# Kernel tuning notes

Hardware: AMD Instinct MI355X
Metric: run time of the kernel (lower is better)

## Reference

```python
import jax, jax.numpy as jnp
import numpy as np

# Kernel codes matching style 'L;O2;P2;Y2,1,1;R0.5;W1,1'
KERNEL_CODES = ['L', 'O', 'P', 'Y', 'R', 'W']
SM_TEMP = 1.0


def _norm_sq(q, k):
    # q: [n,l,h,e], k: [n,s,h,e] -> [n,h,l,s]
    q2 = jnp.einsum('nlhe,nlhe->nhl', q, q)[..., None]        # [n,h,l,1]
    k2 = jnp.einsum('nshe,nshe->nhs', k, k)[:, :, None, :]     # [n,h,1,s]
    qk = jnp.einsum('nlhe,nshe->nhls', q, k)
    return q2 + k2 - 2.0 * qk


def _kernel(code, q, k):
    if code == 'L':
        return jnp.einsum('nlhe,nshe->nhls', q, k)
    if code == 'O':  # -log(1 + ns^(p/2)), p=2
        return -jnp.log1p(_norm_sq(q, k))
    if code == 'P':  # -(ns)^(p/2), p=2
        return -_norm_sq(q, k)
    if code == 'Y':  # (alpha*<q,k> + c)^p, p=2, alpha=1, c=1
        d = jnp.einsum('nlhe,nshe->nhls', q, k)
        return (d + 1.0) ** 2
    if code == 'R':  # exp(-gamma*ns), gamma=0.5
        return jnp.exp(-0.5 * _norm_sq(q, k))
    if code == 'W':  # cos(ns/a)*exp(-ns/b), a=b=1
        ns = _norm_sq(q, k)
        return jnp.cos(ns) * jnp.exp(-ns)
    raise ValueError(code)


def setup_inputs() -> dict:
    key = jax.random.key(0)
    k1, k2, k3, k4 = jax.random.split(key, 4)
    N, L, S, H, E, K = 2, 1024, 1024, 8, 64, 6
    return {
        'query': jax.random.normal(k1, (N, L, H, E), dtype=jnp.float32),
        'key': jax.random.normal(k2, (N, S, H, E), dtype=jnp.float32),
        'attn_mask_add': jnp.zeros((N, L, S), dtype=jnp.float32),
        'key_lengths_add': jnp.zeros((N, S), dtype=jnp.float32),
        'M': jax.random.uniform(k3, (H, E, K), dtype=jnp.float32),
        'C': jax.random.uniform(k4, (K, H, E, E), dtype=jnp.float32),
    }


def reference(query, key, attn_mask_add, key_lengths_add, M, C):
    # mixture weights pi: [n,l,h,k]
    pi = jax.nn.softmax(jnp.einsum('nlhe,hek->nlhk', query, M), axis=-1)
    out = None
    for c, code in enumerate(KERNEL_CODES):
        # htilde = tanh(query @ C[c]): [n,l,h,e]
        htilde = jnp.tanh(jnp.einsum('nlhe,hef->nlhf', query, C[c]))
        qk = _kernel(code, htilde, key)                    # [n,h,l,s]
        qk = qk + attn_mask_add[:, None] + key_lengths_add[:, None, None, :]
        sm = jax.nn.softmax(SM_TEMP * qk, axis=-1)
        w = jnp.transpose(pi[..., c], (0, 2, 1))[..., None]  # [n,h,l,1]
        term = sm * w
        out = term if out is None else out + term
    return out
```

## Files before the change

kernel.cpp:

```cpp
#include <hip/hip_runtime.h>
#include <hip/hip_bf16.h>
#include <math.h>

#define N_  2
#define H_  8
#define G_  16
#define L_  1024
#define S_  1024
#define E_  64
#define NC_ 6

typedef __attribute__((ext_vector_type(4))) float floatx4;
typedef __attribute__((ext_vector_type(8))) short short8;

#define MFMA16 __builtin_amdgcn_mfma_f32_16x16x32_bf16

#define AHAT_OFF   0
#define AHAT_BYTES (NC_*G_*L_*128*2)
#define KHAT_OFF   (AHAT_OFF + AHAT_BYTES)
#define KHAT_BYTES (G_*S_*128*2)
#define PI_OFF     (KHAT_OFF + KHAT_BYTES)
#define PI_BYTES   (NC_*G_*L_*4)
#define HSQ_OFF    (PI_OFF + PI_BYTES)
#define HSQ_BYTES  (NC_*G_*L_*4)
#define KSQ_OFF    (HSQ_OFF + HSQ_BYTES)
#define KSQ_BYTES  (G_*S_*4)

__device__ __forceinline__ float ftanh(float x) {
  return 1.0f - 2.0f * __builtin_amdgcn_rcpf(__expf(2.0f*x) + 1.0f);
}

__global__ __launch_bounds__(256) void k_prep(
    const float* __restrict__ q, const float* __restrict__ C,
    const float* __restrict__ key, const float* __restrict__ M,
    __hip_bfloat16* __restrict__ Ahat, float* __restrict__ hsq,
    __hip_bfloat16* __restrict__ Khat, float* __restrict__ ksq,
    float* __restrict__ pi_t) {
  __shared__ float Ms[384];
  const int bx = blockIdx.x;
  const int t = threadIdx.x;
  const int w = t >> 6, lane = t & 63;
  const int quad = lane >> 4, lc = lane & 15;

  if (bx < 512) {
    const int g = bx >> 5, lch = bx & 31;
    const int n = g >> 3, h = g & 7;
    const int lt = lch*32 + (w >> 1)*16;
    const int c0 = (w & 1)*3;

    short8 qh[2], ql[2];
    #pragma unroll
    for (int kc = 0; kc < 2; kc++) {
      const float* qp = q + (((size_t)(n*L_ + lt + lc))*H_ + h)*E_ + kc*32 + quad*8;
      float4 a0 = *(const float4*)qp, a1 = *(const float4*)(qp + 4);
      float v[8] = {a0.x,a0.y,a0.z,a0.w,a1.x,a1.y,a1.z,a1.w};
      #pragma unroll
      for (int j = 0; j < 8; j++) {
        __hip_bfloat16 hb = __float2bfloat16(v[j]);
        __hip_bfloat16 lb = __float2bfloat16(v[j] - __bfloat162float(hb));
        short hs, ls;
        __builtin_memcpy(&hs, &hb, 2); __builtin_memcpy(&ls, &lb, 2);
        qh[kc][j] = hs; ql[kc][j] = ls;
      }
    }

    #pragma unroll 1
    for (int cc = 0; cc < 3; cc++) {
      const int c = c0 + cc;
      const float* Cb = C + ((size_t)(c*8 + h))*64*64;
      float ss[4] = {0.f, 0.f, 0.f, 0.f};
      #pragma unroll 2
      for (int ft = 0; ft < 4; ft++) {
        short8 bh[2], bl[2];
        #pragma unroll
        for (int kc = 0; kc < 2; kc++)
          #pragma unroll
          for (int j = 0; j < 8; j++) {
            float cv = Cb[(size_t)(kc*32 + quad*8 + j)*64 + ft*16 + lc];
            __hip_bfloat16 hb = __float2bfloat16(cv);
            __hip_bfloat16 lb = __float2bfloat16(cv - __bfloat162float(hb));
            short hs, ls;
            __builtin_memcpy(&hs, &hb, 2); __builtin_memcpy(&ls, &lb, 2);
            bh[kc][j] = hs; bl[kc][j] = ls;
          }
        floatx4 d = {0.f, 0.f, 0.f, 0.f};
        d = MFMA16(qh[0], bh[0], d, 0,0,0);
        d = MFMA16(qh[1], bh[1], d, 0,0,0);
        d = MFMA16(qh[0], bl[0], d, 0,0,0);
        d = MFMA16(qh[1], bl[1], d, 0,0,0);
        d = MFMA16(ql[0], bh[0], d, 0,0,0);
        d = MFMA16(ql[1], bh[1], d, 0,0,0);
        #pragma unroll
        for (int i = 0; i < 4; i++) {
          float hv = ftanh(d[i]);
          ss[i] += hv*hv;
          __hip_bfloat16 hb = __float2bfloat16(hv);
          __hip_bfloat16 lb = __float2bfloat16(hv - __bfloat162float(hb));
          char* rowp = (char*)Ahat +
              (((size_t)(c*G_ + g))*L_ + lt + quad*4 + i)*256;
          *(__hip_bfloat16*)(rowp + (ft*16 + lc)*2)       = hb;
          *(__hip_bfloat16*)(rowp + 128 + (ft*16 + lc)*2) = lb;
        }
      }
      #pragma unroll
      for (int i = 0; i < 4; i++) {
        float s = ss[i];
        s += __shfl_xor(s, 1); s += __shfl_xor(s, 2);
        s += __shfl_xor(s, 4); s += __shfl_xor(s, 8);
        if (lc == 0) hsq[((size_t)(c*G_ + g))*L_ + lt + quad*4 + i] = s;
      }
    }
  } else if (bx < 768) {
    const int kb = bx - 512;
    #pragma unroll 2
    for (int it = 0; it < 16; it++) {
      int r = kb*64 + it*4 + w;
      int kg = r >> 10, s = r & 1023, kn = kg >> 3, kh = kg & 7;
      float v = key[(((size_t)(kn*S_ + s))*H_ + kh)*E_ + lane];
      __hip_bfloat16 hi = __float2bfloat16(v);
      __hip_bfloat16 lo = __float2bfloat16(v - __bfloat162float(hi));
      size_t base = ((size_t)kg*S_ + s)*128;
      Khat[base + lane]      = hi;
      Khat[base + 64 + lane] = lo;
      float sq = v*v;
      #pragma unroll
      for (int off = 32; off; off >>= 1) sq += __shfl_xor(sq, off);
      if (lane == 0) ksq[(size_t)kg*S_ + s] = sq;
    }
  } else {
    const int pb = bx - 768;
    const int pg = pb >> 2, lch = pb & 3;
    const int pn = pg >> 3, ph = pg & 7;
    const int l = lch*256 + t;
    for (int u = t; u < 384; u += 256) Ms[u] = M[ph*384 + u];
    __syncthreads();
    const float* qrow = q + (((size_t)(pn*L_ + l))*H_ + ph)*E_;
    float p[6] = {0.f, 0.f, 0.f, 0.f, 0.f, 0.f};
    #pragma unroll 8
    for (int e = 0; e < 64; e++) {
      float qv = qrow[e];
      #pragma unroll
      for (int k = 0; k < 6; k++) p[k] = fmaf(qv, Ms[e*6 + k], p[k]);
    }
    float mx = p[0];
    #pragma unroll
    for (int k = 1; k < 6; k++) mx = fmaxf(mx, p[k]);
    float den = 0.f;
    #pragma unroll
    for (int k = 0; k < 6; k++) den += __expf(p[k] - mx);
    float rden = __builtin_amdgcn_rcpf(den);
    #pragma unroll
    for (int k = 0; k < 6; k++)
      pi_t[((size_t)(k*G_ + pg))*L_ + l] = __expf(p[k] - mx) * rden;
  }
}

#define LDS_A6LO  0
#define LDS_ZRED  13824
#define LDS_MRED  15360
#define LDS_CST   16896
#define LDS_TOTAL 17664

__global__ __launch_bounds__(256, 2) void k_main(
    const __hip_bfloat16* __restrict__ Ahat, const __hip_bfloat16* __restrict__ Khat,
    const float* __restrict__ hsq, const float* __restrict__ ksq,
    const float* __restrict__ mask, const float* __restrict__ klen,
    const float* __restrict__ pi_t, float* __restrict__ out) {
  extern __shared__ char smraw[];
  char*   A6     = smraw + LDS_A6LO;
  float*  zred   = (float*)(smraw + LDS_ZRED);
  float*  mred   = (float*)(smraw + LDS_MRED);
  float2* cst    = (float2*)(smraw + LDS_CST);

  const int l0 = blockIdx.x * 16; const int g = blockIdx.y; const int n = g >> 3;
  const int t = threadIdx.x; const int w = t >> 6; const int lane = t & 63;
  const int quad = lane >> 4; const int lc = lane & 15;

  #pragma unroll
  for (int rep = 0; rep < 3; rep++) {
    int u = t + rep*256; int row = u >> 3, seg = u & 7;
    int cc = row >> 4, lr = row & 15;
    *(int4*)(A6 + row*144 + seg*16) =
      *(const int4*)((const char*)Ahat +
          (((size_t)(cc*G_ + g))*L_ + l0 + lr)*256 + 128 + seg*16);
  }

  short8 ah[6][2];
  #pragma unroll
  for (int cc = 0; cc < 6; cc++) {
    const char* arow = (const char*)Ahat + (((size_t)(cc*G_ + g))*L_ + l0 + lc)*256;
    ah[cc][0] = *(const short8*)(arow + quad*16);
    ah[cc][1] = *(const short8*)(arow + 64 + quad*16);
  }

  float h1p = 1.0f  + hsq[((size_t)(1*G_ + g))*L_ + l0 + lc];
  float nh2 = 64.0f - hsq[((size_t)(2*G_ + g))*L_ + l0 + lc];
  float h4h = -0.5f * hsq[((size_t)(4*G_ + g))*L_ + l0 + lc];
  float nh5 = -hsq[((size_t)(5*G_ + g))*L_ + l0 + lc];

  __syncthreads();

  auto LOADK = [&](int st, short8 (&bf)[4]) {
    const char* base = (const char*)Khat +
        (((size_t)g)*S_ + st*64 + w*16 + lc)*256 + quad*16;
    #pragma unroll
    for (int kt = 0; kt < 4; kt++)
      bf[kt] = *(const short8*)(base + kt*64);
  };

  float Zc0 = 0.f, Zc1 = 0.f, Zc2 = 0.f, Zc3 = 0.f, zp = 0.f;
  float m3 = -INFINITY, z3 = 0.f;

  auto SWEEP1 = [&](int st, const short8 (&bf)[4]) {
    int sb = st*64 + w*16 + quad*4;
    float4 mk4 = *(const float4*)(mask + ((size_t)(n*L_ + l0 + lc))*S_ + sb);
    float4 kl4 = *(const float4*)(klen + (size_t)n*S_ + sb);
    float4 kq4 = *(const float4*)(ksq  + (size_t)g*S_ + sb);
    float kq[4] = {kq4.x, kq4.y, kq4.z, kq4.w};
    float mv[4], Ev[4];
    mv[0] = mk4.x + kl4.x; mv[1] = mk4.y + kl4.y;
    mv[2] = mk4.z + kl4.z; mv[3] = mk4.w + kl4.w;
    #pragma unroll
    for (int i = 0; i < 4; i++) Ev[i] = __expf(mv[i]);
    #pragma unroll
    for (int c = 0; c < 6; c++) {
      short8 al0 = *(const short8*)(A6 + (c*16 + lc)*144 + quad*16);
      short8 al1 = *(const short8*)(A6 + (c*16 + lc)*144 + 64 + quad*16);
      floatx4 a = {0.f, 0.f, 0.f, 0.f};
      a = MFMA16(bf[0], ah[c][0], a, 0,0,0);
      a = MFMA16(bf[1], ah[c][1], a, 0,0,0);
      a = MFMA16(bf[0], al0,      a, 0,0,0);
      a = MFMA16(bf[1], al1,      a, 0,0,0);
      a = MFMA16(bf[2], ah[c][0], a, 0,0,0);
      a = MFMA16(bf[3], ah[c][1], a, 0,0,0);
      #pragma unroll
      for (int i = 0; i < 4; i++) {
        float d = a[i];
        if (c == 0) {
          Zc0 = fmaf(Ev[i], __expf(d), Zc0);
        } else if (c == 1) {
          Zc1 = fmaf(Ev[i], __builtin_amdgcn_rcpf(fmaf(-2.f, d, h1p + kq[i])), Zc1);
        } else if (c == 2) {
          zp += __expf(fmaf(2.f, d, nh2 - kq[i] + mv[i]));
        } else if (c == 3) {
          float tt = d + 1.f;
          float x  = fmaf(tt, tt, mv[i]);
          float mn = fmaxf(m3, x);
          float e  = __expf(fminf(m3, x) - mn);
          z3 = (x > m3) ? fmaf(z3, e, 1.0f) : (z3 + e);
          m3 = mn;
        } else if (c == 4) {
          Zc2 = fmaf(Ev[i], __expf(__expf(d + fmaf(-0.5f, kq[i], h4h))), Zc2);
        } else {
          float a5 = fmaf(2.f, d, nh5 - kq[i]);
          Zc3 = fmaf(Ev[i], __expf(__cosf(a5) * __expf(a5)), Zc3);
        }
      }
    }
  };

  {
    short8 bA[4], bB[4];
    LOADK(0, bA);
    #pragma unroll 1
    for (int st = 0; st < 16; st += 2) {
      LOADK(st + 1, bB);
      SWEEP1(st, bA);
      LOADK((st + 2) & 15, bA);
      SWEEP1(st + 1, bB);
    }
  }

  #pragma unroll
  for (int off = 16; off < 64; off <<= 1) {
    Zc0 += __shfl_xor(Zc0, off); Zc1 += __shfl_xor(Zc1, off);
    Zc2 += __shfl_xor(Zc2, off); Zc3 += __shfl_xor(Zc3, off);
    zp  += __shfl_xor(zp,  off);
    float mo = __shfl_xor(m3, off);
    float zo = __shfl_xor(z3, off);
    float mn = fmaxf(m3, mo);
    float e  = __expf(fminf(m3, mo) - mn);
    z3 = (mo > m3) ? fmaf(z3, e, zo) : fmaf(zo, e, z3);
    m3 = mn;
  }
  if (lane < 16) {
    zred[w*96 + 0*16 + lc] = Zc0; mred[w*96 + 0*16 + lc] = 0.f;
    zred[w*96 + 1*16 + lc] = Zc1; mred[w*96 + 1*16 + lc] = 0.f;
    zred[w*96 + 2*16 + lc] = zp;  mred[w*96 + 2*16 + lc] = 0.f;
    zred[w*96 + 3*16 + lc] = z3;  mred[w*96 + 3*16 + lc] = m3;
    zred[w*96 + 4*16 + lc] = Zc2; mred[w*96 + 4*16 + lc] = 0.f;
    zred[w*96 + 5*16 + lc] = Zc3; mred[w*96 + 5*16 + lc] = 0.f;
  }
  __syncthreads();
  if (t < 96) {
    int c = t >> 4;
    float z = zred[t], m = mred[t];
    if (c == 3) {
      #pragma unroll
      for (int w2 = 1; w2 < 4; w2++) {
        float mo = mred[w2*96 + t], zo = zred[w2*96 + t];
        float mn = fmaxf(m, mo);
        float e  = __expf(fminf(m, mo) - mn);
        z = (mo > m) ? fmaf(z, e, zo) : fmaf(zo, e, z);
        m = mn;
      }
    } else {
      #pragma unroll
      for (int w2 = 1; w2 < 4; w2++) z += zred[w2*96 + t];
    }
    float piv = pi_t[((size_t)((t >> 4)*G_ + g))*L_ + l0 + (t & 15)];
    cst[t] = make_float2(piv / z, m);
  }
  __syncthreads();

  float ac0 = cst[0*16 + lc].x, ac1 = cst[1*16 + lc].x, ac2 = cst[2*16 + lc].x;
  float ac3 = cst[3*16 + lc].x, ac4 = cst[4*16 + lc].x, ac5 = cst[5*16 + lc].x;
  float m3f = cst[3*16 + lc].y;

  auto SWEEP2 = [&](int st, const short8 (&bf)[4]) {
    int sb = st*64 + w*16 + quad*4;
    float4 mk4 = *(const float4*)(mask + ((size_t)(n*L_ + l0 + lc))*S_ + sb);
    float4 kl4 = *(const float4*)(klen + (size_t)n*S_ + sb);
    float4 kq4 = *(const float4*)(ksq  + (size_t)g*S_ + sb);
    float kq[4] = {kq4.x, kq4.y, kq4.z, kq4.w};
    float mv[4], Ev[4];
    mv[0] = mk4.x + kl4.x; mv[1] = mk4.y + kl4.y;
    mv[2] = mk4.z + kl4.z; mv[3] = mk4.w + kl4.w;
    #pragma unroll
    for (int i = 0; i < 4; i++) Ev[i] = __expf(mv[i]);
    float Sacc[4] = {0.f, 0.f, 0.f, 0.f};
    float Gg[4]   = {0.f, 0.f, 0.f, 0.f};
    #pragma unroll
    for (int c = 0; c < 6; c++) {
      short8 al0 = *(const short8*)(A6 + (c*16 + lc)*144 + quad*16);
      short8 al1 = *(const short8*)(A6 + (c*16 + lc)*144 + 64 + quad*16);
      floatx4 a = {0.f, 0.f, 0.f, 0.f};
      a = MFMA16(bf[0], ah[c][0], a, 0,0,0);
      a = MFMA16(bf[1], ah[c][1], a, 0,0,0);
      a = MFMA16(bf[0], al0,      a, 0,0,0);
      a = MFMA16(bf[1], al1,      a, 0,0,0);
      a = MFMA16(bf[2], ah[c][0], a, 0,0,0);
      a = MFMA16(bf[3], ah[c][1], a, 0,0,0);
      #pragma unroll
      for (int i = 0; i < 4; i++) {
        float d = a[i];
        if (c == 0) {
          Sacc[i] = fmaf(ac0, __expf(d), Sacc[i]);
        } else if (c == 1) {
          Sacc[i] = fmaf(ac1, __builtin_amdgcn_rcpf(fmaf(-2.f, d, h1p + kq[i])), Sacc[i]);
        } else if (c == 2) {
          Gg[i] = fmaf(ac2, __expf(fmaf(2.f, d, nh2 - kq[i] + mv[i])), Gg[i]);
        } else if (c == 3) {
          float tt = d + 1.f;
          float x  = fmaf(tt, tt, mv[i]);
          Gg[i] = fmaf(ac3, __expf(x - m3f), Gg[i]);
        } else if (c == 4) {
          Sacc[i] = fmaf(ac4, __expf(__expf(d + fmaf(-0.5f, kq[i], h4h))), Sacc[i]);
        } else {
          float a5 = fmaf(2.f, d, nh5 - kq[i]);
          Sacc[i] = fmaf(ac5, __expf(__cosf(a5) * __expf(a5)), Sacc[i]);
        }
      }
    }
    float4 ov;
    ov.x = fmaf(Ev[0], Sacc[0], Gg[0]);
    ov.y = fmaf(Ev[1], Sacc[1], Gg[1]);
    ov.z = fmaf(Ev[2], Sacc[2], Gg[2]);
    ov.w = fmaf(Ev[3], Sacc[3], Gg[3]);
    *(float4*)(out + (((size_t)g)*L_ + l0 + lc)*S_ + sb) = ov;
  };

  {
    short8 bA[4], bB[4];
    LOADK(0, bA);
    #pragma unroll 1
    for (int st = 0; st < 16; st += 2) {
      LOADK(st + 1, bB);
      SWEEP2(st, bA);
      LOADK((st + 2) & 15, bA);
      SWEEP2(st + 1, bB);
    }
  }
}

extern "C" void kernel_launch(void* const* d_in, const int* in_sizes, int n_in,
                              void* d_out, int out_size, void* d_ws, size_t ws_size,
                              hipStream_t stream) {
  (void)in_sizes; (void)n_in; (void)out_size; (void)ws_size;
  const float* q    = (const float*)d_in[0];
  const float* key  = (const float*)d_in[1];
  const float* mask = (const float*)d_in[2];
  const float* klen = (const float*)d_in[3];
  const float* M    = (const float*)d_in[4];
  const float* C    = (const float*)d_in[5];
  char* ws = (char*)d_ws;
  __hip_bfloat16* Ahat = (__hip_bfloat16*)(ws + AHAT_OFF);
  __hip_bfloat16* Khat = (__hip_bfloat16*)(ws + KHAT_OFF);
  float* pi_t    = (float*)(ws + PI_OFF);
  float* hsq     = (float*)(ws + HSQ_OFF);
  float* ksq     = (float*)(ws + KSQ_OFF);
  float* out = (float*)d_out;

  k_prep<<<832, 256, 0, stream>>>(q, C, key, M, Ahat, hsq, Khat, ksq, pi_t);
  k_main<<<dim3(64, 16), 256, LDS_TOTAL, stream>>>(Ahat, Khat, hsq, ksq, mask, klen,
                                                   pi_t, out);
}
```

Measured before the change: 207.2 us.

## Move A hi/lo fragments to LDS, premerge mask+klen, raise occupancy to three blocks

The hi bf16 query fragments now live in LDS together with the lo parts, which frees registers, and launch bounds go from 2 to 3 blocks per CU. A new prep stage precomputes mask+key_length into a workspace buffer, so the main kernel does one load instead of two and folds the additive mask into the exponent instead of multiplying by exp(mask). The K-tile double buffer is replaced by a single buffer that is prefetched after the last MFMA. The costs are extra LDS reads per tile, an extra 8 MB write and read of the merged mask, and less latency hiding from the single buffer.

```diff
diff --git a/kernel.cpp b/kernel.cpp
--- a/kernel.cpp
+++ b/kernel.cpp
@@ -25,6 +25,8 @@
 #define HSQ_BYTES  (NC_*G_*L_*4)
 #define KSQ_OFF    (HSQ_OFF + HSQ_BYTES)
 #define KSQ_BYTES  (G_*S_*4)
+#define MKL_OFF    (KSQ_OFF + KSQ_BYTES)
+#define MKL_BYTES  (N_*L_*S_*4)
 
 __device__ __forceinline__ float ftanh(float x) {
   return 1.0f - 2.0f * __builtin_amdgcn_rcpf(__expf(2.0f*x) + 1.0f);
@@ -33,9 +35,10 @@
 __global__ __launch_bounds__(256) void k_prep(
     const float* __restrict__ q, const float* __restrict__ C,
     const float* __restrict__ key, const float* __restrict__ M,
+    const float* __restrict__ mask, const float* __restrict__ klen,
     __hip_bfloat16* __restrict__ Ahat, float* __restrict__ hsq,
     __hip_bfloat16* __restrict__ Khat, float* __restrict__ ksq,
-    float* __restrict__ pi_t) {
+    float* __restrict__ pi_t, float* __restrict__ mkl) {
   __shared__ float Ms[384];
   const int bx = blockIdx.x;
   const int t = threadIdx.x;
@@ -127,7 +130,7 @@
       for (int off = 32; off; off >>= 1) sq += __shfl_xor(sq, off);
       if (lane == 0) ksq[(size_t)kg*S_ + s] = sq;
     }
-  } else {
+  } else if (bx < 832) {
     const int pb = bx - 768;
     const int pg = pb >> 2, lch = pb & 3;
     const int pn = pg >> 3, ph = pg & 7;
@@ -152,45 +155,49 @@
     #pragma unroll
     for (int k = 0; k < 6; k++)
       pi_t[((size_t)(k*G_ + pg))*L_ + l] = __expf(p[k] - mx) * rden;
+  } else {
+    const int mb = bx - 832;
+    const float4* m4 = (const float4*)mask;
+    const float4* k4 = (const float4*)klen;
+    float4* o4 = (float4*)mkl;
+    #pragma unroll 1
+    for (int u = mb*256 + t; u < N_*L_*S_/4; u += 128*256) {
+      int nn = u >> 18;
+      int s4 = u & 255;
+      float4 a = m4[u], b = k4[nn*256 + s4];
+      o4[u] = make_float4(a.x+b.x, a.y+b.y, a.z+b.z, a.w+b.w);
+    }
   }
 }
 
-#define LDS_A6LO  0
-#define LDS_ZRED  13824
-#define LDS_MRED  15360
-#define LDS_CST   16896
-#define LDS_TOTAL 17664
-
-__global__ __launch_bounds__(256, 2) void k_main(
+#define LDS_A6    0
+#define LDS_ZRED  26112
+#define LDS_MRED  27648
+#define LDS_CST   29184
+#define LDS_TOTAL 29952
+
+__global__ __launch_bounds__(256, 3) void k_main(
     const __hip_bfloat16* __restrict__ Ahat, const __hip_bfloat16* __restrict__ Khat,
     const float* __restrict__ hsq, const float* __restrict__ ksq,
-    const float* __restrict__ mask, const float* __restrict__ klen,
-    const float* __restrict__ pi_t, float* __restrict__ out) {
+    const float* __restrict__ mkl, const float* __restrict__ pi_t,
+    float* __restrict__ out) {
   extern __shared__ char smraw[];
-  char*   A6     = smraw + LDS_A6LO;
-  float*  zred   = (float*)(smraw + LDS_ZRED);
-  float*  mred   = (float*)(smraw + LDS_MRED);
-  float2* cst    = (float2*)(smraw + LDS_CST);
+  char*   A6   = smraw + LDS_A6;
+  float*  zred = (float*)(smraw + LDS_ZRED);
+  float*  mred = (float*)(smraw + LDS_MRED);
+  float2* cst  = (float2*)(smraw + LDS_CST);
 
   const int l0 = blockIdx.x * 16; const int g = blockIdx.y; const int n = g >> 3;
   const int t = threadIdx.x; const int w = t >> 6; const int lane = t & 63;
   const int quad = lane >> 4; const int lc = lane & 15;
 
   #pragma unroll
-  for (int rep = 0; rep < 3; rep++) {
-    int u = t + rep*256; int row = u >> 3, seg = u & 7;
+  for (int rep = 0; rep < 6; rep++) {
+    int u = t + rep*256; int row = u >> 4, seg = u & 15;
     int cc = row >> 4, lr = row & 15;
-    *(int4*)(A6 + row*144 + seg*16) =
+    *(int4*)(A6 + row*272 + seg*16) =
       *(const int4*)((const char*)Ahat +
-          (((size_t)(cc*G_ + g))*L_ + l0 + lr)*256 + 128 + seg*16);
-  }
-
-  short8 ah[6][2];
-  #pragma unroll
-  for (int cc = 0; cc < 6; cc++) {
-    const char* arow = (const char*)Ahat + (((size_t)(cc*G_ + g))*L_ + l0 + lc)*256;
-    ah[cc][0] = *(const short8*)(arow + quad*16);
-    ah[cc][1] = *(const short8*)(arow + 64 + quad*16);
+          (((size_t)(cc*G_ + g))*L_ + l0 + lr)*256 + seg*16);
   }
 
   float h1p = 1.0f  + hsq[((size_t)(1*G_ + g))*L_ + l0 + lc];
@@ -211,63 +218,56 @@
   float Zc0 = 0.f, Zc1 = 0.f, Zc2 = 0.f, Zc3 = 0.f, zp = 0.f;
   float m3 = -INFINITY, z3 = 0.f;
 
-  auto SWEEP1 = [&](int st, const short8 (&bf)[4]) {
-    int sb = st*64 + w*16 + quad*4;
-    float4 mk4 = *(const float4*)(mask + ((size_t)(n*L_ + l0 + lc))*S_ + sb);
-    float4 kl4 = *(const float4*)(klen + (size_t)n*S_ + sb);
-    float4 kq4 = *(const float4*)(ksq  + (size_t)g*S_ + sb);
-    float kq[4] = {kq4.x, kq4.y, kq4.z, kq4.w};
-    float mv[4], Ev[4];
-    mv[0] = mk4.x + kl4.x; mv[1] = mk4.y + kl4.y;
-    mv[2] = mk4.z + kl4.z; mv[3] = mk4.w + kl4.w;
-    #pragma unroll
-    for (int i = 0; i < 4; i++) Ev[i] = __expf(mv[i]);
-    #pragma unroll
-    for (int c = 0; c < 6; c++) {
-      short8 al0 = *(const short8*)(A6 + (c*16 + lc)*144 + quad*16);
-      short8 al1 = *(const short8*)(A6 + (c*16 + lc)*144 + 64 + quad*16);
-      floatx4 a = {0.f, 0.f, 0.f, 0.f};
-      a = MFMA16(bf[0], ah[c][0], a, 0,0,0);
-      a = MFMA16(bf[1], ah[c][1], a, 0,0,0);
-      a = MFMA16(bf[0], al0,      a, 0,0,0);
-      a = MFMA16(bf[1], al1,      a, 0,0,0);
-      a = MFMA16(bf[2], ah[c][0], a, 0,0,0);
-      a = MFMA16(bf[3], ah[c][1], a, 0,0,0);
-      #pragma unroll
-      for (int i = 0; i < 4; i++) {
-        float d = a[i];
-        if (c == 0) {
-          Zc0 = fmaf(Ev[i], __expf(d), Zc0);
-        } else if (c == 1) {
-          Zc1 = fmaf(Ev[i], __builtin_amdgcn_rcpf(fmaf(-2.f, d, h1p + kq[i])), Zc1);
-        } else if (c == 2) {
-          zp += __expf(fmaf(2.f, d, nh2 - kq[i] + mv[i]));
-        } else if (c == 3) {
-          float tt = d + 1.f;
-          float x  = fmaf(tt, tt, mv[i]);
-          float mn = fmaxf(m3, x);
-          float e  = __expf(fminf(m3, x) - mn);
-          z3 = (x > m3) ? fmaf(z3, e, 1.0f) : (z3 + e);
-          m3 = mn;
-        } else if (c == 4) {
-          Zc2 = fmaf(Ev[i], __expf(__expf(d + fmaf(-0.5f, kq[i], h4h))), Zc2);
-        } else {
-          float a5 = fmaf(2.f, d, nh5 - kq[i]);
-          Zc3 = fmaf(Ev[i], __expf(__cosf(a5) * __expf(a5)), Zc3);
+  {
+    short8 bf[4];
+    LOADK(0, bf);
+    #pragma unroll 1
+    for (int st = 0; st < 16; st++) {
+      int sb = st*64 + w*16 + quad*4;
+      float4 mv4 = *(const float4*)(mkl + ((size_t)(n*L_ + l0 + lc))*S_ + sb);
+      float4 kq4 = *(const float4*)(ksq + (size_t)g*S_ + sb);
+      float mv[4] = {mv4.x, mv4.y, mv4.z, mv4.w};
+      float kq[4] = {kq4.x, kq4.y, kq4.z, kq4.w};
+      #pragma unroll
+      for (int c = 0; c < 6; c++) {
+        const char* Ar = A6 + (c*16 + lc)*272 + quad*16;
+        short8 h0  = *(const short8*)(Ar);
+        short8 h1  = *(const short8*)(Ar + 64);
+        short8 al0 = *(const short8*)(Ar + 128);
+        short8 al1 = *(const short8*)(Ar + 192);
+        floatx4 a = {0.f, 0.f, 0.f, 0.f};
+        a = MFMA16(bf[0], h0,  a, 0,0,0);
+        a = MFMA16(bf[1], h1,  a, 0,0,0);
+        a = MFMA16(bf[0], al0, a, 0,0,0);
+        a = MFMA16(bf[1], al1, a, 0,0,0);
+        a = MFMA16(bf[2], h0,  a, 0,0,0);
+        a = MFMA16(bf[3], h1,  a, 0,0,0);
+        if (c == 5) LOADK((st + 1) & 15, bf);
+        #pragma unroll
+        for (int i = 0; i < 4; i++) {
+          float d = a[i];
+          if (c == 0) {
+            Zc0 += __expf(d + mv[i]);
+          } else if (c == 1) {
+            Zc1 = fmaf(__expf(mv[i]),
+                __builtin_amdgcn_rcpf(fmaf(-2.f, d, h1p + kq[i])), Zc1);
+          } else if (c == 2) {
+            zp += __expf(fmaf(2.f, d, nh2 - kq[i] + mv[i]));
+          } else if (c == 3) {
+            float tt = d + 1.f;
+            float x  = fmaf(tt, tt, mv[i]);
+            float mn = fmaxf(m3, x);
+            float e  = __expf(fminf(m3, x) - mn);
+            z3 = (x > m3) ? fmaf(z3, e, 1.0f) : (z3 + e);
+            m3 = mn;
+          } else if (c == 4) {
+            Zc2 += __expf(__expf(d + fmaf(-0.5f, kq[i], h4h)) + mv[i]);
+          } else {
+            float a5 = fmaf(2.f, d, nh5 - kq[i]);
+            Zc3 += __expf(fmaf(__cosf(a5), __expf(a5), mv[i]));
+          }
         }
       }
-    }
-  };
-
-  {
-    short8 bA[4], bB[4];
-    LOADK(0, bA);
-    #pragma unroll 1
-    for (int st = 0; st < 16; st += 2) {
-      LOADK(st + 1, bB);
-      SWEEP1(st, bA);
-      LOADK((st + 2) & 15, bA);
-      SWEEP1(st + 1, bB);
     }
   }
 
@@ -317,68 +317,57 @@
   float ac3 = cst[3*16 + lc].x, ac4 = cst[4*16 + lc].x, ac5 = cst[5*16 + lc].x;
   float m3f = cst[3*16 + lc].y;
 
-  auto SWEEP2 = [&](int st, const short8 (&bf)[4]) {
-    int sb = st*64 + w*16 + quad*4;
-    float4 mk4 = *(const float4*)(mask + ((size_t)(n*L_ + l0 + lc))*S_ + sb);
-    float4 kl4 = *(const float4*)(klen + (size_t)n*S_ + sb);
-    float4 kq4 = *(const float4*)(ksq  + (size_t)g*S_ + sb);
-    float kq[4] = {kq4.x, kq4.y, kq4.z, kq4.w};
-    float mv[4], Ev[4];
-    mv[0] = mk4.x + kl4.x; mv[1] = mk4.y + kl4.y;
-    mv[2] = mk4.z + kl4.z; mv[3] = mk4.w + kl4.w;
-    #pragma unroll
-    for (int i = 0; i < 4; i++) Ev[i] = __expf(mv[i]);
-    float Sacc[4] = {0.f, 0.f, 0.f, 0.f};
-    float Gg[4]   = {0.f, 0.f, 0.f, 0.f};
-    #pragma unroll
-    for (int c = 0; c < 6; c++) {
-      short8 al0 = *(const short8*)(A6 + (c*16 + lc)*144 + quad*16);
-      short8 al1 = *(const short8*)(A6 + (c*16 + lc)*144 + 64 + quad*16);
-      floatx4 a = {0.f, 0.f, 0.f, 0.f};
-      a = MFMA16(bf[0], ah[c][0], a, 0,0,0);
-      a = MFMA16(bf[1], ah[c][1], a, 0,0,0);
-      a = MFMA16(bf[0], al0,      a, 0,0,0);
-      a = MFMA16(bf[1], al1,      a, 0,0,0);
-      a = MFMA16(bf[2], ah[c][0], a, 0,0,0);
-      a = MFMA16(bf[3], ah[c][1], a, 0,0,0);
-      #pragma unroll
-      for (int i = 0; i < 4; i++) {
-        float d = a[i];
-        if (c == 0) {
-          Sacc[i] = fmaf(ac0, __expf(d), Sacc[i]);
-        } else if (c == 1) {
-          Sacc[i] = fmaf(ac1, __builtin_amdgcn_rcpf(fmaf(-2.f, d, h1p + kq[i])), Sacc[i]);
-        } else if (c == 2) {
-          Gg[i] = fmaf(ac2, __expf(fmaf(2.f, d, nh2 - kq[i] + mv[i])), Gg[i]);
-        } else if (c == 3) {
-          float tt = d + 1.f;
-          float x  = fmaf(tt, tt, mv[i]);
-          Gg[i] = fmaf(ac3, __expf(x - m3f), Gg[i]);
-        } else if (c == 4) {
-          Sacc[i] = fmaf(ac4, __expf(__expf(d + fmaf(-0.5f, kq[i], h4h))), Sacc[i]);
-        } else {
-          float a5 = fmaf(2.f, d, nh5 - kq[i]);
-          Sacc[i] = fmaf(ac5, __expf(__cosf(a5) * __expf(a5)), Sacc[i]);
+  {
+    short8 bf[4];
+    LOADK(0, bf);
+    #pragma unroll 1
+    for (int st = 0; st < 16; st++) {
+      int sb = st*64 + w*16 + quad*4;
+      float4 mv4 = *(const float4*)(mkl + ((size_t)(n*L_ + l0 + lc))*S_ + sb);
+      float4 kq4 = *(const float4*)(ksq + (size_t)g*S_ + sb);
+      float mv[4] = {mv4.x, mv4.y, mv4.z, mv4.w};
+      float kq[4] = {kq4.x, kq4.y, kq4.z, kq4.w};
+      float Gg[4] = {0.f, 0.f, 0.f, 0.f};
+      #pragma unroll
+      for (int c = 0; c < 6; c++) {
+        const char* Ar = A6 + (c*16 + lc)*272 + quad*16;
+        short8 h0  = *(const short8*)(Ar);
+        short8 h1  = *(const short8*)(Ar + 64);
+        short8 al0 = *(const short8*)(Ar + 128);
+        short8 al1 = *(const short8*)(Ar + 192);
+        floatx4 a = {0.f, 0.f, 0.f, 0.f};
+        a = MFMA16(bf[0], h0,  a, 0,0,0);
+        a = MFMA16(bf[1], h1,  a, 0,0,0);
+        a = MFMA16(bf[0], al0, a, 0,0,0);
+        a = MFMA16(bf[1], al1, a, 0,0,0);
+        a = MFMA16(bf[2], h0,  a, 0,0,0);
+        a = MFMA16(bf[3], h1,  a, 0,0,0);
+        if (c == 5) LOADK((st + 1) & 15, bf);
+        #pragma unroll
+        for (int i = 0; i < 4; i++) {
+          float d = a[i];
+          if (c == 0) {
+            Gg[i] = fmaf(ac0, __expf(d + mv[i]), Gg[i]);
+          } else if (c == 1) {
+            Gg[i] = fmaf(ac1 * __expf(mv[i]),
+                __builtin_amdgcn_rcpf(fmaf(-2.f, d, h1p + kq[i])), Gg[i]);
+          } else if (c == 2) {
+            Gg[i] = fmaf(ac2, __expf(fmaf(2.f, d, nh2 - kq[i] + mv[i])), Gg[i]);
+          } else if (c == 3) {
+            float tt = d + 1.f;
+            Gg[i] = fmaf(ac3, __expf(fmaf(tt, tt, mv[i]) - m3f), Gg[i]);
+          } else if (c == 4) {
+            Gg[i] = fmaf(ac4,
+                __expf(__expf(d + fmaf(-0.5f, kq[i], h4h)) + mv[i]), Gg[i]);
+          } else {
+            float a5 = fmaf(2.f, d, nh5 - kq[i]);
+            Gg[i] = fmaf(ac5, __expf(fmaf(__cosf(a5), __expf(a5), mv[i])), Gg[i]);
+          }
         }
       }
-    }
-    float4 ov;
-    ov.x = fmaf(Ev[0], Sacc[0], Gg[0]);
-    ov.y = fmaf(Ev[1], Sacc[1], Gg[1]);
-    ov.z = fmaf(Ev[2], Sacc[2], Gg[2]);
-    ov.w = fmaf(Ev[3], Sacc[3], Gg[3]);
-    *(float4*)(out + (((size_t)g)*L_ + l0 + lc)*S_ + sb) = ov;
-  };
-
-  {
-    short8 bA[4], bB[4];
-    LOADK(0, bA);
-    #pragma unroll 1
-    for (int st = 0; st < 16; st += 2) {
-      LOADK(st + 1, bB);
-      SWEEP2(st, bA);
-      LOADK((st + 2) & 15, bA);
-      SWEEP2(st + 1, bB);
+      float4 ov;
+      ov.x = Gg[0]; ov.y = Gg[1]; ov.z = Gg[2]; ov.w = Gg[3];
+      *(float4*)(out + (((size_t)g)*L_ + l0 + lc)*S_ + sb) = ov;
     }
   }
 }
@@ -399,9 +388,11 @@
   float* pi_t    = (float*)(ws + PI_OFF);
   float* hsq     = (float*)(ws + HSQ_OFF);
   float* ksq     = (float*)(ws + KSQ_OFF);
+  float* mkl     = (float*)(ws + MKL_OFF);
   float* out = (float*)d_out;
 
-  k_prep<<<832, 256, 0, stream>>>(q, C, key, M, Ahat, hsq, Khat, ksq, pi_t);
-  k_main<<<dim3(64, 16), 256, LDS_TOTAL, stream>>>(Ahat, Khat, hsq, ksq, mask, klen,
+  k_prep<<<960, 256, 0, stream>>>(q, C, key, M, mask, klen,
+                                  Ahat, hsq, Khat, ksq, pi_t, mkl);
+  k_main<<<dim3(64, 16), 256, LDS_TOTAL, stream>>>(Ahat, Khat, hsq, ksq, mkl,
                                                    pi_t, out);
 }
```

After: 221.0 us. 6.7% more time.

## Precombine mask and key-length bias in prep and prefetch them with key tiles

Applied to the files above, without the earlier changes.

Adds a prep stage that sums attn_mask and key_lengths into an mkl buffer, so the main kernel reads one bias array instead of two. The bias and ksq loads are now software-pipelined alongside the K tile prefetch. Each wave also starts its S sweep at a different tile offset, which spreads concurrent accesses across memory. The cost is an extra 8MB write and read through the workspace in the prep kernel, to save one small load and an add per element in the two main sweeps.

```diff
diff --git a/kernel.cpp b/kernel.cpp
--- a/kernel.cpp
+++ b/kernel.cpp
@@ -25,6 +25,8 @@
 #define HSQ_BYTES  (NC_*G_*L_*4)
 #define KSQ_OFF    (HSQ_OFF + HSQ_BYTES)
 #define KSQ_BYTES  (G_*S_*4)
+#define MKL_OFF    (KSQ_OFF + KSQ_BYTES)
+#define MKL_BYTES  (N_*L_*S_*4)
 
 __device__ __forceinline__ float ftanh(float x) {
   return 1.0f - 2.0f * __builtin_amdgcn_rcpf(__expf(2.0f*x) + 1.0f);
@@ -33,9 +35,10 @@
 __global__ __launch_bounds__(256) void k_prep(
     const float* __restrict__ q, const float* __restrict__ C,
     const float* __restrict__ key, const float* __restrict__ M,
+    const float* __restrict__ mask, const float* __restrict__ klen,
     __hip_bfloat16* __restrict__ Ahat, float* __restrict__ hsq,
     __hip_bfloat16* __restrict__ Khat, float* __restrict__ ksq,
-    float* __restrict__ pi_t) {
+    float* __restrict__ pi_t, float* __restrict__ mkl) {
   __shared__ float Ms[384];
   const int bx = blockIdx.x;
   const int t = threadIdx.x;
@@ -127,7 +130,7 @@
       for (int off = 32; off; off >>= 1) sq += __shfl_xor(sq, off);
       if (lane == 0) ksq[(size_t)kg*S_ + s] = sq;
     }
-  } else {
+  } else if (bx < 832) {
     const int pb = bx - 768;
     const int pg = pb >> 2, lch = pb & 3;
     const int pn = pg >> 3, ph = pg & 7;
@@ -152,6 +155,18 @@
     #pragma unroll
     for (int k = 0; k < 6; k++)
       pi_t[((size_t)(k*G_ + pg))*L_ + l] = __expf(p[k] - mx) * rden;
+  } else {
+    const int mb = bx - 832;
+    const float4* m4 = (const float4*)mask;
+    const float4* k4 = (const float4*)klen;
+    float4* o4 = (float4*)mkl;
+    #pragma unroll 1
+    for (int u = mb*256 + t; u < N_*L_*S_/4; u += 128*256) {
+      int nn = u >> 18;
+      int s4 = u & 255;
+      float4 a = m4[u], b = k4[nn*256 + s4];
+      o4[u] = make_float4(a.x+b.x, a.y+b.y, a.z+b.z, a.w+b.w);
+    }
   }
 }
 
@@ -164,13 +179,13 @@
 __global__ __launch_bounds__(256, 2) void k_main(
     const __hip_bfloat16* __restrict__ Ahat, const __hip_bfloat16* __restrict__ Khat,
     const float* __restrict__ hsq, const float* __restrict__ ksq,
-    const float* __restrict__ mask, const float* __restrict__ klen,
-    const float* __restrict__ pi_t, float* __restrict__ out) {
+    const float* __restrict__ mkl, const float* __restrict__ pi_t,
+    float* __restrict__ out) {
   extern __shared__ char smraw[];
-  char*   A6     = smraw + LDS_A6LO;
-  float*  zred   = (float*)(smraw + LDS_ZRED);
-  float*  mred   = (float*)(smraw + LDS_MRED);
-  float2* cst    = (float2*)(smraw + LDS_CST);
+  char*   A6   = smraw + LDS_A6LO;
+  float*  zred = (float*)(smraw + LDS_ZRED);
+  float*  mred = (float*)(smraw + LDS_MRED);
+  float2* cst  = (float2*)(smraw + LDS_CST);
 
   const int l0 = blockIdx.x * 16; const int g = blockIdx.y; const int n = g >> 3;
   const int t = threadIdx.x; const int w = t >> 6; const int lane = t & 63;
@@ -207,19 +222,21 @@
     for (int kt = 0; kt < 4; kt++)
       bf[kt] = *(const short8*)(base + kt*64);
   };
+  auto LOADS = [&](int st, float4& mv4, float4& kq4) {
+    int sb = st*64 + w*16 + quad*4;
+    mv4 = *(const float4*)(mkl + ((size_t)(n*L_ + l0 + lc))*S_ + sb);
+    kq4 = *(const float4*)(ksq + (size_t)g*S_ + sb);
+  };
+
+  const int sbase = w*4;
 
   float Zc0 = 0.f, Zc1 = 0.f, Zc2 = 0.f, Zc3 = 0.f, zp = 0.f;
   float m3 = -INFINITY, z3 = 0.f;
 
-  auto SWEEP1 = [&](int st, const short8 (&bf)[4]) {
-    int sb = st*64 + w*16 + quad*4;
-    float4 mk4 = *(const float4*)(mask + ((size_t)(n*L_ + l0 + lc))*S_ + sb);
-    float4 kl4 = *(const float4*)(klen + (size_t)n*S_ + sb);
-    float4 kq4 = *(const float4*)(ksq  + (size_t)g*S_ + sb);
+  auto SWEEP1 = [&](const short8 (&bf)[4], const float4 mv4, const float4 kq4) {
     float kq[4] = {kq4.x, kq4.y, kq4.z, kq4.w};
-    float mv[4], Ev[4];
-    mv[0] = mk4.x + kl4.x; mv[1] = mk4.y + kl4.y;
-    mv[2] = mk4.z + kl4.z; mv[3] = mk4.w + kl4.w;
+    float mv[4] = {mv4.x, mv4.y, mv4.z, mv4.w};
+    float Ev[4];
     #pragma unroll
     for (int i = 0; i < 4; i++) Ev[i] = __expf(mv[i]);
     #pragma unroll
@@ -261,13 +278,16 @@
 
   {
     short8 bA[4], bB[4];
-    LOADK(0, bA);
+    float4 mvA, kqA, mvB, kqB;
+    LOADK(sbase & 15, bA); LOADS(sbase & 15, mvA, kqA);
     #pragma unroll 1
-    for (int st = 0; st < 16; st += 2) {
-      LOADK(st + 1, bB);
-      SWEEP1(st, bA);
-      LOADK((st + 2) & 15, bA);
-      SWEEP1(st + 1, bB);
+    for (int k = 0; k < 16; k += 2) {
+      int stB = (sbase + k + 1) & 15;
+      int stC = (sbase + k + 2) & 15;
+      LOADK(stB, bB); LOADS(stB, mvB, kqB);
+      SWEEP1(bA, mvA, kqA);
+      LOADK(stC, bA); LOADS(stC, mvA, kqA);
+      SWEEP1(bB, mvB, kqB);
     }
   }
 
@@ -317,15 +337,11 @@
   float ac3 = cst[3*16 + lc].x, ac4 = cst[4*16 + lc].x, ac5 = cst[5*16 + lc].x;
   float m3f = cst[3*16 + lc].y;
 
-  auto SWEEP2 = [&](int st, const short8 (&bf)[4]) {
-    int sb = st*64 + w*16 + quad*4;
-    float4 mk4 = *(const float4*)(mask + ((size_t)(n*L_ + l0 + lc))*S_ + sb);
-    float4 kl4 = *(const float4*)(klen + (size_t)n*S_ + sb);
-    float4 kq4 = *(const float4*)(ksq  + (size_t)g*S_ + sb);
+  auto SWEEP2 = [&](int st, const short8 (&bf)[4],
+                    const float4 mv4, const float4 kq4) {
     float kq[4] = {kq4.x, kq4.y, kq4.z, kq4.w};
-    float mv[4], Ev[4];
-    mv[0] = mk4.x + kl4.x; mv[1] = mk4.y + kl4.y;
-    mv[2] = mk4.z + kl4.z; mv[3] = mk4.w + kl4.w;
+    float mv[4] = {mv4.x, mv4.y, mv4.z, mv4.w};
+    float Ev[4];
     #pragma unroll
     for (int i = 0; i < 4; i++) Ev[i] = __expf(mv[i]);
     float Sacc[4] = {0.f, 0.f, 0.f, 0.f};
@@ -367,18 +383,23 @@
     ov.y = fmaf(Ev[1], Sacc[1], Gg[1]);
     ov.z = fmaf(Ev[2], Sacc[2], Gg[2]);
     ov.w = fmaf(Ev[3], Sacc[3], Gg[3]);
+    int sb = st*64 + w*16 + quad*4;
     *(float4*)(out + (((size_t)g)*L_ + l0 + lc)*S_ + sb) = ov;
   };
 
   {
     short8 bA[4], bB[4];
-    LOADK(0, bA);
+    float4 mvA, kqA, mvB, kqB;
+    LOADK(sbase & 15, bA); LOADS(sbase & 15, mvA, kqA);
     #pragma unroll 1
-    for (int st = 0; st < 16; st += 2) {
-      LOADK(st + 1, bB);
-      SWEEP2(st, bA);
-      LOADK((st + 2) & 15, bA);
-      SWEEP2(st + 1, bB);
+    for (int k = 0; k < 16; k += 2) {
+      int stA = (sbase + k) & 15;
+      int stB = (sbase + k + 1) & 15;
+      int stC = (sbase + k + 2) & 15;
+      LOADK(stB, bB); LOADS(stB, mvB, kqB);
+      SWEEP2(stA, bA, mvA, kqA);
+      LOADK(stC, bA); LOADS(stC, mvA, kqA);
+      SWEEP2(stB, bB, mvB, kqB);
     }
   }
 }
@@ -399,9 +420,11 @@
   float* pi_t    = (float*)(ws + PI_OFF);
   float* hsq     = (float*)(ws + HSQ_OFF);
   float* ksq     = (float*)(ws + KSQ_OFF);
+  float* mkl     = (float*)(ws + MKL_OFF);
   float* out = (float*)d_out;
 
-  k_prep<<<832, 256, 0, stream>>>(q, C, key, M, Ahat, hsq, Khat, ksq, pi_t);
-  k_main<<<dim3(64, 16), 256, LDS_TOTAL, stream>>>(Ahat, Khat, hsq, ksq, mask, klen,
+  k_prep<<<960, 256, 0, stream>>>(q, C, key, M, mask, klen,
+                                  Ahat, hsq, Khat, ksq, pi_t, mkl);
+  k_main<<<dim3(64, 16), 256, LDS_TOTAL, stream>>>(Ahat, Khat, hsq, ksq, mkl,
                                                    pi_t, out);
 }
```

Result: no change. 209.5 us (+1.1%).
